# Optimization experiments

Measured on AMD Instinct MI355X. Metric: run time of the kernel, lower is better.

## Reference

```python
import jax, jax.numpy as jnp
import numpy as np

H = 128        # hidden_dim
HEADS = 4      # conv1 heads
NTYPE = 50     # node_type_num
MZN = 32       # model_zoo_num
MAXN = 64      # max_node_num
B = 16         # outer batch
G = B * MZN    # num graphs = 512
N = G * MAXN   # total nodes = 32768
E = N * 8      # edges = 262144


def layer_norm(x, g, b):
    mu = x.mean(-1, keepdims=True)
    var = ((x - mu) ** 2).mean(-1, keepdims=True)
    return (x - mu) / jnp.sqrt(var + 1e-6) * g + b


def gat_conv(x, src, dst, W, a_src, a_dst, bias):
    # PyG GATConv: lin (no bias) -> per-edge LeakyReLU(0.2) scores with
    # self-loops -> segment softmax over dst -> scatter-sum, concat heads + bias.
    n = x.shape[0]
    heads, c = a_src.shape
    xp = (x @ W).reshape(n, heads, c)              # [N,heads,c]
    al_s = (xp * a_src).sum(-1)                    # [N,heads]
    al_d = (xp * a_dst).sum(-1)                    # [N,heads]
    loop = jnp.arange(n)
    s = jnp.concatenate([src, loop])               # add self-loops
    d = jnp.concatenate([dst, loop])
    e = jax.nn.leaky_relu(al_s[s] + al_d[d], 0.2)  # [E+N,heads]
    m = jax.ops.segment_max(e, d, num_segments=n)
    ex = jnp.exp(e - m[d])
    denom = jax.ops.segment_sum(ex, d, num_segments=n)
    alpha = ex / denom[d]                          # segment softmax
    msg = xp[s] * alpha[:, :, None]                # [E+N,heads,c]
    out = jax.ops.segment_sum(msg, d, num_segments=n)
    return out.reshape(n, heads * c) + bias


def setup_inputs() -> dict:
    key = jax.random.key(0)
    ks = jax.random.split(key, 32)
    def rn(k, shape, s=0.05):
        return jax.random.normal(k, shape, jnp.float32) * s
    inp = {
        "t": jax.random.normal(ks[0], (G, 768), jnp.float32),
        "v": jax.random.normal(ks[1], (G, 768), jnp.float32),
        "m_idx": jax.random.randint(ks[2], (N,), 0, NTYPE + 1),
        "edge_index": jax.random.randint(ks[3], (2, E), 0, N),
        "Wt": rn(ks[4], (768, H)), "bt": jnp.zeros((H,), jnp.float32),
        "Wv": rn(ks[5], (768, H)), "bv": jnp.zeros((H,), jnp.float32),
        "emb": rn(ks[6], (NTYPE + 1, H), 1.0),
        "Wnode": rn(ks[7], (H, H)), "bnode": jnp.zeros((H,), jnp.float32),
        "Wstart": rn(ks[8], (2 * H, H)), "bstart": jnp.zeros((H,), jnp.float32),
        "ln_g": jnp.ones((H,), jnp.float32), "ln_b": jnp.zeros((H,), jnp.float32),
        "W1": rn(ks[9], (H, HEADS * H)),
        "a_src1": rn(ks[10], (HEADS, H)), "a_dst1": rn(ks[11], (HEADS, H)),
        "b1": jnp.zeros((HEADS * H,), jnp.float32),
        "W2": rn(ks[12], (HEADS * H, H)),
        "a_src2": rn(ks[13], (1, H)), "a_dst2": rn(ks[14], (1, H)),
        "b2": jnp.zeros((H,), jnp.float32),
        "Wo1": rn(ks[15], (H, H)), "bo1": jnp.zeros((H,), jnp.float32),
        "Wo2": rn(ks[16], (H, 1)), "bo2": jnp.zeros((1,), jnp.float32),
    }
    return inp


def reference(t, v, Wt, bt, Wv, bv, emb, Wnode, bnode, Wstart, bstart, ln_g, ln_b,
              W1, a_src1, a_dst1, b1, W2, a_src2, a_dst2, b2, Wo1, bo1, Wo2, bo2,
              m_idx, edge_index):
    te = t @ Wt + bt                               # [G,H]
    ve = v @ Wv + bv                               # [G,H]
    ne = emb[m_idx].reshape(G, MAXN, H)            # node type embeddings
    ne = ne @ Wnode + bnode
    start = jnp.concatenate([ve, te], axis=-1) @ Wstart + bstart
    ne = ne.at[:, 0].set(start).reshape(N, H)
    x = layer_norm(ne, ln_g, ln_b)
    src, dst = edge_index[0], edge_index[1]
    x = jax.nn.elu(gat_conv(x, src, dst, W1, a_src1, a_dst1, b1))  # [N,4H]
    x = jax.nn.elu(gat_conv(x, src, dst, W2, a_src2, a_dst2, b2))  # [N,H]
    mask = (m_idx >= 1).astype(x.dtype).reshape(G, MAXN, 1)
    pooled = (x.reshape(G, MAXN, H) * mask).sum(1) / mask.sum(1)   # masked mean
    h1 = jax.nn.leaky_relu(pooled.reshape(B, MZN, H) @ Wo1 + bo1, 0.01)
    logits = (h1 @ Wo2 + bo2).reshape(B, MZN)
    return logits
```

## Files before the change

### kernel.cpp

```cpp
#include <hip/hip_runtime.h>
#include <hip/hip_bf16.h>

typedef __hip_bfloat16 bf16;
typedef __attribute__((ext_vector_type(8))) short s8v;
typedef __attribute__((ext_vector_type(4))) float f4v;

#define NN 32768
#define EE 262144
#define GG 512
#define LDW 520

__device__ __forceinline__ float2 unpk(unsigned u) {
  float2 r;
  r.x = __uint_as_float(u << 16);
  r.y = __uint_as_float(u & 0xffff0000u);
  return r;
}
__device__ __forceinline__ unsigned pk(float x, float y) {
  union { bf16 h[2]; unsigned u; } p;
  p.h[0] = __float2bfloat16(x);
  p.h[1] = __float2bfloat16(y);
  return p.u;
}
__device__ __forceinline__ short f2bf_bits(float x) {
  bf16 h = __float2bfloat16(x);
  return *reinterpret_cast<short*>(&h);
}
__device__ __forceinline__ float wred_sum(float v) {
#pragma unroll
  for (int o = 32; o; o >>= 1) v += __shfl_xor(v, o, 64);
  return v;
}

__device__ __forceinline__ void packB_one(const float* W, int N, int K, int id, s8v* Bp) {
  int lane = id & 63;
  int tmp = id >> 6;
  int ksteps = K >> 5;
  int ks = tmp % ksteps;
  int nt = tmp / ksteps;
  int n = nt * 16 + (lane & 15);
  int kbase = ks * 32 + (lane >> 4) * 8;
  s8v r;
#pragma unroll
  for (int j = 0; j < 8; j++) r[j] = f2bf_bits(W[(size_t)(kbase + j) * N + n]);
  Bp[id] = r;
}

__global__ __launch_bounds__(256) void prep_kernel(
    const int* __restrict__ dst, int* __restrict__ indeg,
    const float* __restrict__ W1, s8v* __restrict__ Bp1,
    const float* __restrict__ W2, s8v* __restrict__ Bp2,
    const float* __restrict__ a_src1, const float* __restrict__ a_dst1,
    float* __restrict__ ws1, float* __restrict__ wd1,
    const float* __restrict__ emb, const float* __restrict__ Wnode,
    const float* __restrict__ bnode, bf16* __restrict__ emb2_b,
    const float* __restrict__ Wv, const float* __restrict__ Wt,
    const float* __restrict__ Ws,
    const float* __restrict__ bv, const float* __restrict__ bt,
    const float* __restrict__ bstart,
    float* __restrict__ Wvs, float* __restrict__ Wts,
    float* __restrict__ bs2) {
  int b = blockIdx.x, tid = threadIdx.x;
  if (b < 1024) {
    int e = b * 256 + tid;
    atomicAdd(&indeg[dst[e]], 1);
  } else if (b < 1056) {
    packB_one(W1, 512, 128, (b - 1024) * 256 + tid, Bp1);
  } else if (b < 1088) {
    packB_one(W2, 128, 512, (b - 1056) * 256 + tid, Bp2);
  } else if (b < 1090) {
    int id = (b - 1088) * 256 + tid;
    int h = id >> 7, k = id & 127;
    float s = 0.f, d = 0.f;
    for (int c = 0; c < 128; c++) {
      float w0 = W1[(size_t)k * 512 + h * 128 + c];
      s = fmaf(w0, a_src1[h * 128 + c], s);
      d = fmaf(w0, a_dst1[h * 128 + c], d);
    }
    ws1[id] = s;
    wd1[id] = d;
  } else if (b < 1192) {
    __shared__ float red[256];
    int bb = b - 1090;
    int lo = tid & 63, slice = tid >> 6;
    long oid = (long)bb * 64 + lo;
    bool live = (oid < 51L * 128);
    int m = 0, n = 0;
    if (live) { m = (int)(oid >> 7); n = (int)(oid & 127); }
    float acc = 0.f;
    if (live) {
      const float* Ar = emb + (size_t)m * 128;
      for (int k = slice * 32; k < slice * 32 + 32; k++)
        acc = fmaf(Ar[k], Wnode[(size_t)k * 128 + n], acc);
    }
    red[tid] = acc;
    __syncthreads();
    if (slice == 0 && live) {
      float v = red[lo] + red[64 + lo] + red[128 + lo] + red[192 + lo];
      emb2_b[(size_t)m * 128 + n] = __float2bfloat16(v + bnode[n]);
    }
  } else if (b < 1576) {
    int id = (b - 1192) * 256 + tid;
    bool isT = id >= 49152;
    int o = isT ? id - 49152 : id;
    int k = o >> 6, cp = o & 63, c0 = cp * 2;
    const float* Wrow = (isT ? Wt : Wv) + (size_t)k * 128;
    const float* Wsc = Ws + (isT ? (size_t)128 * 128 : 0);
    float s0 = 0.f, s1 = 0.f;
    for (int j = 0; j < 128; j++) {
      float w = Wrow[j];
      float2 q = *(const float2*)(Wsc + (size_t)j * 128 + c0);
      s0 = fmaf(w, q.x, s0);
      s1 = fmaf(w, q.y, s1);
    }
    float* dp = (isT ? Wts : Wvs) + (size_t)k * 128 + c0;
    dp[0] = s0;
    dp[1] = s1;
  } else {
    if (tid < 128) {
      float s = bstart[tid];
      for (int k = 0; k < 128; k++) {
        s = fmaf(bv[k], Ws[(size_t)k * 128 + tid], s);
        s = fmaf(bt[k], Ws[(size_t)(128 + k) * 128 + tid], s);
      }
      bs2[tid] = s;
    }
  }
}

__global__ __launch_bounds__(1024) void scan_start_kernel(
    const int* __restrict__ indeg, int* __restrict__ off, int* __restrict__ cursor,
    const float* __restrict__ tf, const float* __restrict__ vf,
    const float* __restrict__ Wvs, const float* __restrict__ Wts,
    const float* __restrict__ bs2, bf16* __restrict__ start_b) {
  int t = threadIdx.x;
  if (blockIdx.x == 0) {
    __shared__ int sh[1024];
    int loc[32];
    int s = 0;
    int base = t * 32;
#pragma unroll
    for (int j = 0; j < 32; j++) { loc[j] = indeg[base + j]; s += loc[j]; }
    sh[t] = s;
    __syncthreads();
    for (int d = 1; d < 1024; d <<= 1) {
      int v = (t >= d) ? sh[t - d] : 0;
      __syncthreads();
      sh[t] += v;
      __syncthreads();
    }
    int run = (t == 0) ? 0 : sh[t - 1];
#pragma unroll
    for (int j = 0; j < 32; j++) { off[base + j] = run; cursor[base + j] = run; run += loc[j]; }
    if (t == 1023) off[NN] = run;
    return;
  }
  __shared__ float red[1024];
  int g = blockIdx.x - 1;
  int c = t & 127, slice = t >> 7;
  const float* vrow = vf + (size_t)g * 768;
  const float* trow = tf + (size_t)g * 768;
  float acc = 0.f;
  int k0 = slice * 96;
#pragma unroll 4
  for (int k = k0; k < k0 + 96; k++)
    acc = fmaf(vrow[k], Wvs[(size_t)k * 128 + c], fmaf(trow[k], Wts[(size_t)k * 128 + c], acc));
  red[t] = acc;
  __syncthreads();
  if (t < 512) red[t] += red[t + 512];
  __syncthreads();
  if (t < 256) red[t] += red[t + 256];
  __syncthreads();
  if (t < 128) {
    float s = red[t] + red[t + 128] + bs2[t];
    start_b[(size_t)g * 128 + t] = __float2bfloat16(s);
  }
}

__global__ __launch_bounds__(256) void fill_ln_kernel(
    const int* __restrict__ src, const int* __restrict__ dst,
    int* __restrict__ cursor, int* __restrict__ esrc,
    const unsigned* __restrict__ start_b, const unsigned* __restrict__ emb2_b,
    const int* __restrict__ m_idx, const float* __restrict__ lng,
    const float* __restrict__ lnb, const float* __restrict__ ws1,
    const float* __restrict__ wd1, unsigned* __restrict__ x0b,
    float* __restrict__ als, float* __restrict__ ald) {
  int b = blockIdx.x;
  if (b < 1024) {
    int e = b * 256 + threadIdx.x;
    int p = atomicAdd(&cursor[dst[e]], 1);
    esrc[p] = src[e];
    return;
  }
  int bb = b - 1024;
  int i = bb * 4 + (threadIdx.x >> 6);
  int lane = threadIdx.x & 63;
  int g = i >> 6, n = i & 63;
  const unsigned* row = (n == 0) ? (start_b + (size_t)g * 64) : (emb2_b + (size_t)m_idx[i] * 64);
  float2 v = unpk(row[lane]);
  float mu = wred_sum(v.x + v.y) * (1.f / 128.f);
  float dx = v.x - mu, dy = v.y - mu;
  float var = wred_sum(dx * dx + dy * dy) * (1.f / 128.f);
  float rstd = rsqrtf(var + 1e-6f);
  float2 gg = ((const float2*)lng)[lane];
  float2 bbv = ((const float2*)lnb)[lane];
  float xx = dx * rstd * gg.x + bbv.x;
  float xy = dy * rstd * gg.y + bbv.y;
  x0b[(size_t)i * 64 + lane] = pk(xx, xy);
#pragma unroll
  for (int h = 0; h < 4; h++) {
    float2 s2 = ((const float2*)(ws1 + h * 128))[lane];
    float2 d2 = ((const float2*)(wd1 + h * 128))[lane];
    float ps = wred_sum(xx * s2.x + xy * s2.y);
    float pd = wred_sum(xx * d2.x + xy * d2.y);
    if (lane == 0) { als[i * 4 + h] = ps; ald[i * 4 + h] = pd; }
  }
}

__global__ __launch_bounds__(256) void alpha1_kernel(const float4* __restrict__ als4,
                                                     const float4* __restrict__ ald4,
                                                     const int* __restrict__ off,
                                                     const int* __restrict__ esrc,
                                                     float4* __restrict__ aw4,
                                                     float4* __restrict__ selfw4,
                                                     float4* __restrict__ inv4) {
  int i = blockIdx.x * 256 + threadIdx.x;
  if (i >= NN) return;
  float4 ad = ald4[i];
  float4 as = als4[i];
  float4 sw;
  {
    float v0 = as.x + ad.x, v1 = as.y + ad.y, v2 = as.z + ad.z, v3 = as.w + ad.w;
    v0 = v0 > 0.f ? v0 : 0.2f * v0; v1 = v1 > 0.f ? v1 : 0.2f * v1;
    v2 = v2 > 0.f ? v2 : 0.2f * v2; v3 = v3 > 0.f ? v3 : 0.2f * v3;
    sw = make_float4(__expf(v0), __expf(v1), __expf(v2), __expf(v3));
  }
  float d0 = sw.x, d1 = sw.y, d2 = sw.z, d3 = sw.w;
  int s0 = off[i], s1 = off[i + 1];
  for (int e = s0; e < s1; e++) {
    float4 a = als4[esrc[e]];
    float v0 = a.x + ad.x, v1 = a.y + ad.y, v2 = a.z + ad.z, v3 = a.w + ad.w;
    v0 = v0 > 0.f ? v0 : 0.2f * v0; v1 = v1 > 0.f ? v1 : 0.2f * v1;
    v2 = v2 > 0.f ? v2 : 0.2f * v2; v3 = v3 > 0.f ? v3 : 0.2f * v3;
    v0 = __expf(v0); v1 = __expf(v1); v2 = __expf(v2); v3 = __expf(v3);
    aw4[e] = make_float4(v0, v1, v2, v3);
    d0 += v0; d1 += v1; d2 += v2; d3 += v3;
  }
  selfw4[i] = sw;
  inv4[i] = make_float4(1.f / d0, 1.f / d1, 1.f / d2, 1.f / d3);
}

__global__ __launch_bounds__(256) void alpha2_kernel(const float* __restrict__ als,
                                                     const float* __restrict__ ald,
                                                     const int* __restrict__ off,
                                                     const int* __restrict__ esrc,
                                                     float* __restrict__ aw,
                                                     float* __restrict__ selfw,
                                                     float* __restrict__ inv) {
  int i = blockIdx.x * 256 + threadIdx.x;
  if (i >= NN) return;
  float adi = ald[i];
  float selfSc = als[i] + adi;
  selfSc = selfSc > 0.f ? selfSc : 0.2f * selfSc;
  float sw = __expf(selfSc);
  float denom = sw;
  int s0 = off[i], s1 = off[i + 1];
  for (int e = s0; e < s1; e++) {
    float sc = als[esrc[e]] + adi;
    sc = sc > 0.f ? sc : 0.2f * sc;
    float w = __expf(sc);
    aw[e] = w;
    denom += w;
  }
  selfw[i] = sw;
  inv[i] = 1.f / denom;
}

__global__ __launch_bounds__(256) void conv12f_kernel(
    const uint4* __restrict__ x0,
    const float4* __restrict__ aw4, const float4* __restrict__ selfw4,
    const float4* __restrict__ inv4,
    const int* __restrict__ off, const int* __restrict__ esrc,
    const s8v* __restrict__ Bp1, const float* __restrict__ b1,
    const s8v* __restrict__ Bp2,
    const float* __restrict__ a_src2, const float* __restrict__ a_dst2,
    short* __restrict__ xp2, float* __restrict__ als2, float* __restrict__ ald2) {
  __shared__ short lds[64 * LDW];
  int tid = threadIdx.x;
  int brow = blockIdx.x * 64;
  {
    int c8 = tid & 15, rsub = tid >> 4;
    for (int grp = 0; grp < 4; grp++) {
      int i = brow + grp * 16 + rsub;
      float4 sw = selfw4[i];
      uint4 xv = x0[(size_t)i * 16 + c8];
      float x[8];
      { float2 p0 = unpk(xv.x), p1 = unpk(xv.y), p2 = unpk(xv.z), p3 = unpk(xv.w);
        x[0]=p0.x; x[1]=p0.y; x[2]=p1.x; x[3]=p1.y; x[4]=p2.x; x[5]=p2.y; x[6]=p3.x; x[7]=p3.y; }
      float acc[4][8];
#pragma unroll
      for (int j = 0; j < 8; j++) {
        acc[0][j] = sw.x * x[j]; acc[1][j] = sw.y * x[j];
        acc[2][j] = sw.z * x[j]; acc[3][j] = sw.w * x[j];
      }
      int s0 = off[i], s1 = off[i + 1];
      for (int e = s0; e < s1; e++) {
        int s = esrc[e];
        float4 wv = aw4[e];
        uint4 m = x0[(size_t)s * 16 + c8];
        float2 q0 = unpk(m.x), q1 = unpk(m.y), q2 = unpk(m.z), q3 = unpk(m.w);
        float q[8] = {q0.x, q0.y, q1.x, q1.y, q2.x, q2.y, q3.x, q3.y};
#pragma unroll
        for (int j = 0; j < 8; j++) {
          acc[0][j] = fmaf(wv.x, q[j], acc[0][j]);
          acc[1][j] = fmaf(wv.y, q[j], acc[1][j]);
          acc[2][j] = fmaf(wv.z, q[j], acc[2][j]);
          acc[3][j] = fmaf(wv.w, q[j], acc[3][j]);
        }
      }
      float4 iv = inv4[i];
      float ivh[4] = {iv.x, iv.y, iv.z, iv.w};
      int row = grp * 16 + rsub;
#pragma unroll
      for (int h = 0; h < 4; h++) {
        uint4 o;
        o.x = pk(acc[h][0] * ivh[h], acc[h][1] * ivh[h]);
        o.y = pk(acc[h][2] * ivh[h], acc[h][3] * ivh[h]);
        o.z = pk(acc[h][4] * ivh[h], acc[h][5] * ivh[h]);
        o.w = pk(acc[h][6] * ivh[h], acc[h][7] * ivh[h]);
        *(uint4*)(lds + row * LDW + h * 128 + c8 * 8) = o;
      }
    }
  }
  __syncthreads();
  int wv = tid >> 6, lane = tid & 63, quad = lane >> 4, l16 = lane & 15;
  int arow = (wv * 16 + l16) * LDW;
  for (int h = 0; h < 4; h++) {
    f4v acc[8] = {};
#pragma unroll
    for (int ks = 0; ks < 4; ks++) {
      s8v a = *(const s8v*)(lds + arow + h * 128 + ks * 32 + quad * 8);
#pragma unroll
      for (int nt = 0; nt < 8; nt++) {
        s8v bf = Bp1[(size_t)((h * 8 + nt) * 4 + ks) * 64 + lane];
        acc[nt] = __builtin_amdgcn_mfma_f32_16x16x32_bf16(a, bf, acc[nt], 0, 0, 0);
      }
    }
#pragma unroll
    for (int nt = 0; nt < 8; nt++) {
      float bb = b1[h * 128 + nt * 16 + l16];
#pragma unroll
      for (int r = 0; r < 4; r++) {
        float vv = acc[nt][r] + bb;
        vv = vv > 0.f ? vv : (__expf(vv) - 1.f);
        lds[(wv * 16 + quad * 4 + r) * LDW + h * 128 + nt * 16 + l16] = f2bf_bits(vv);
      }
    }
  }
  __syncthreads();
  f4v acc2[8] = {};
  for (int ks = 0; ks < 16; ks++) {
    s8v a = *(const s8v*)(lds + arow + ks * 32 + quad * 8);
#pragma unroll
    for (int nt = 0; nt < 8; nt++) {
      s8v bf = Bp2[(size_t)(nt * 16 + ks) * 64 + lane];
      acc2[nt] = __builtin_amdgcn_mfma_f32_16x16x32_bf16(a, bf, acc2[nt], 0, 0, 0);
    }
  }
#pragma unroll
  for (int nt = 0; nt < 8; nt++)
#pragma unroll
    for (int r = 0; r < 4; r++)
      lds[(wv * 16 + quad * 4 + r) * LDW + nt * 16 + l16] = f2bf_bits(acc2[nt][r]);
  float2 as = ((const float2*)a_src2)[lane];
  float2 ad = ((const float2*)a_dst2)[lane];
  for (int r = 0; r < 16; r++) {
    int row = wv * 16 + r;
    float2 x = unpk(*(const unsigned*)(lds + row * LDW + lane * 2));
    float ps = wred_sum(x.x * as.x + x.y * as.y);
    float pd = wred_sum(x.x * ad.x + x.y * ad.y);
    if (lane == 0) { als2[brow + row] = ps; ald2[brow + row] = pd; }
  }
  __syncthreads();
#pragma unroll
  for (int rep = 0; rep < 4; rep++) {
    int idx = rep * 256 + tid;
    int row = idx >> 4, c16 = idx & 15;
    uint4 val = *(const uint4*)(lds + row * LDW + c16 * 8);
    *(uint4*)(xp2 + (size_t)(brow + row) * 128 + c16 * 8) = val;
  }
}

__global__ __launch_bounds__(256) void tail2_kernel(
    const uint4* __restrict__ xp,
    const float* __restrict__ aw, const float* __restrict__ selfw,
    const float* __restrict__ inv,
    const int* __restrict__ off, const int* __restrict__ esrc,
    const float* __restrict__ b2, const int* __restrict__ m_idx,
    const float* __restrict__ Wo1, const float* __restrict__ bo1,
    const float* __restrict__ Wo2, const float* __restrict__ bo2,
    float* __restrict__ out) {
  __shared__ float x2t[64 * 132];
  __shared__ float maskf[64];
  __shared__ float pl[128];
  __shared__ float red[256];
  int g = blockIdx.x, tid = threadIdx.x;
  if (tid < 64) maskf[tid] = (m_idx[g * 64 + tid] >= 1) ? 1.f : 0.f;
  int c8 = tid & 15, rsub = tid >> 4;
  for (int grp = 0; grp < 4; grp++) {
    int i = g * 64 + grp * 16 + rsub;
    float sw = selfw[i];
    float ivv = inv[i];
    uint4 xv = xp[(size_t)i * 16 + c8];
    float2 p0 = unpk(xv.x), p1 = unpk(xv.y), p2 = unpk(xv.z), p3 = unpk(xv.w);
    float a0 = sw * p0.x, a1 = sw * p0.y, a2 = sw * p1.x, a3 = sw * p1.y;
    float a4 = sw * p2.x, a5 = sw * p2.y, a6 = sw * p3.x, a7 = sw * p3.y;
    int s0 = off[i], s1 = off[i + 1];
    int e = s0;
    for (; e + 1 < s1; e += 2) {
      int sA = esrc[e], sB = esrc[e + 1];
      float wA = aw[e], wB = aw[e + 1];
      uint4 mA = xp[(size_t)sA * 16 + c8];
      uint4 mB = xp[(size_t)sB * 16 + c8];
      float2 q0 = unpk(mA.x), q1 = unpk(mA.y), q2 = unpk(mA.z), q3 = unpk(mA.w);
      a0 = fmaf(wA, q0.x, a0); a1 = fmaf(wA, q0.y, a1);
      a2 = fmaf(wA, q1.x, a2); a3 = fmaf(wA, q1.y, a3);
      a4 = fmaf(wA, q2.x, a4); a5 = fmaf(wA, q2.y, a5);
      a6 = fmaf(wA, q3.x, a6); a7 = fmaf(wA, q3.y, a7);
      q0 = unpk(mB.x); q1 = unpk(mB.y); q2 = unpk(mB.z); q3 = unpk(mB.w);
      a0 = fmaf(wB, q0.x, a0); a1 = fmaf(wB, q0.y, a1);
      a2 = fmaf(wB, q1.x, a2); a3 = fmaf(wB, q1.y, a3);
      a4 = fmaf(wB, q2.x, a4); a5 = fmaf(wB, q2.y, a5);
      a6 = fmaf(wB, q3.x, a6); a7 = fmaf(wB, q3.y, a7);
    }
    if (e < s1) {
      int sA = esrc[e];
      float wA = aw[e];
      uint4 mA = xp[(size_t)sA * 16 + c8];
      float2 q0 = unpk(mA.x), q1 = unpk(mA.y), q2 = unpk(mA.z), q3 = unpk(mA.w);
      a0 = fmaf(wA, q0.x, a0); a1 = fmaf(wA, q0.y, a1);
      a2 = fmaf(wA, q1.x, a2); a3 = fmaf(wA, q1.y, a3);
      a4 = fmaf(wA, q2.x, a4); a5 = fmaf(wA, q2.y, a5);
      a6 = fmaf(wA, q3.x, a6); a7 = fmaf(wA, q3.y, a7);
    }
    float4 bb0 = ((const float4*)b2)[c8 * 2];
    float4 bb1 = ((const float4*)b2)[c8 * 2 + 1];
    a0 = a0 * ivv + bb0.x; a1 = a1 * ivv + bb0.y; a2 = a2 * ivv + bb0.z; a3 = a3 * ivv + bb0.w;
    a4 = a4 * ivv + bb1.x; a5 = a5 * ivv + bb1.y; a6 = a6 * ivv + bb1.z; a7 = a7 * ivv + bb1.w;
    a0 = a0 > 0.f ? a0 : (__expf(a0) - 1.f);
    a1 = a1 > 0.f ? a1 : (__expf(a1) - 1.f);
    a2 = a2 > 0.f ? a2 : (__expf(a2) - 1.f);
    a3 = a3 > 0.f ? a3 : (__expf(a3) - 1.f);
    a4 = a4 > 0.f ? a4 : (__expf(a4) - 1.f);
    a5 = a5 > 0.f ? a5 : (__expf(a5) - 1.f);
    a6 = a6 > 0.f ? a6 : (__expf(a6) - 1.f);
    a7 = a7 > 0.f ? a7 : (__expf(a7) - 1.f);
    float* dp = x2t + (grp * 16 + rsub) * 132 + c8 * 8;
    dp[0] = a0; dp[1] = a1; dp[2] = a2; dp[3] = a3;
    dp[4] = a4; dp[5] = a5; dp[6] = a6; dp[7] = a7;
  }
  __syncthreads();
  int c = tid & 127, half = tid >> 7;
  float pacc = 0.f;
  for (int n = half * 32; n < half * 32 + 32; n++) pacc += maskf[n] * x2t[n * 132 + c];
  red[tid] = pacc;
  __syncthreads();
  float cnt = 0.f;
  for (int n = 0; n < 64; n++) cnt += maskf[n];
  if (half == 0) pl[c] = (red[c] + red[c + 128]) / cnt;
  __syncthreads();
  float hacc = 0.f;
  for (int k = half * 64; k < half * 64 + 64; k++)
    hacc = fmaf(pl[k], Wo1[(size_t)k * 128 + c], hacc);
  red[tid] = hacc;
  __syncthreads();
  if (half == 0) {
    float hh = red[c] + red[c + 128] + bo1[c];
    hh = hh > 0.f ? hh : 0.01f * hh;
    red[c] = hh * Wo2[c];
  }
  __syncthreads();
  for (int d = 64; d; d >>= 1) {
    if (tid < d) red[tid] += red[tid + d];
    __syncthreads();
  }
  if (tid == 0) out[g] = red[0] + bo2[0];
}

extern "C" void kernel_launch(void* const* d_in, const int* in_sizes, int n_in, void* d_out,
                              int out_size, void* d_ws, size_t ws_size, hipStream_t stream) {
  (void)n_in; (void)out_size; (void)ws_size;
  bool dict_order = (in_sizes[2] == NN);
  int IM, IE, IF[25];
  if (dict_order) {
    IM = 2; IE = 3;
    const int f[25] = {0, 1, 4, 5, 6, 7, 8, 9, 10, 11, 12, 13, 14, 15, 16, 17, 18,
                       19, 20, 21, 22, 23, 24, 25, 26};
    for (int k = 0; k < 25; k++) IF[k] = f[k];
  } else {
    IM = 25; IE = 26;
    for (int k = 0; k < 25; k++) IF[k] = k;
  }
  const int* m_idx = (const int*)d_in[IM];
  const int* eidx = (const int*)d_in[IE];
  float* out = (float*)d_out;
  const int* e_src = eidx;
  const int* e_dst = eidx + EE;

  const float* t = (const float*)d_in[IF[0]];
  const float* v = (const float*)d_in[IF[1]];
  const float* Wt = (const float*)d_in[IF[2]];     const float* bt = (const float*)d_in[IF[3]];
  const float* Wv = (const float*)d_in[IF[4]];     const float* bv = (const float*)d_in[IF[5]];
  const float* emb = (const float*)d_in[IF[6]];
  const float* Wnode = (const float*)d_in[IF[7]];  const float* bnode = (const float*)d_in[IF[8]];
  const float* Wstart = (const float*)d_in[IF[9]]; const float* bstart = (const float*)d_in[IF[10]];
  const float* ln_g = (const float*)d_in[IF[11]];  const float* ln_b = (const float*)d_in[IF[12]];
  const float* W1 = (const float*)d_in[IF[13]];
  const float* a_src1 = (const float*)d_in[IF[14]]; const float* a_dst1 = (const float*)d_in[IF[15]];
  const float* b1 = (const float*)d_in[IF[16]];
  const float* W2 = (const float*)d_in[IF[17]];
  const float* a_src2 = (const float*)d_in[IF[18]]; const float* a_dst2 = (const float*)d_in[IF[19]];
  const float* b2 = (const float*)d_in[IF[20]];
  const float* Wo1 = (const float*)d_in[IF[21]];   const float* bo1 = (const float*)d_in[IF[22]];
  const float* Wo2 = (const float*)d_in[IF[23]];   const float* bo2 = (const float*)d_in[IF[24]];

  char* w = (char*)d_ws;
  bf16* x0b = (bf16*)w;
  bf16* xp2b = (bf16*)(w + ((size_t)8 << 20));
  size_t so = (size_t)16 << 20;
  bf16* emb2_b = (bf16*)(w + so); so += 51 * 128 * 2 + 256;
  bf16* start_b = (bf16*)(w + so); so += 512 * 128 * 2;
  float* als1 = (float*)(w + so); so += NN * 4 * 4;
  float* ald1 = (float*)(w + so); so += NN * 4 * 4;
  float* als2 = (float*)(w + so); so += NN * 4;
  float* ald2 = (float*)(w + so); so += NN * 4;
  float* aw1 = (float*)(w + so); so += EE * 4 * 4;
  float* selfw1 = (float*)(w + so); so += NN * 4 * 4;
  float* inv1 = (float*)(w + so); so += NN * 4 * 4;
  float* aw2 = (float*)(w + so); so += EE * 4;
  float* selfw2 = (float*)(w + so); so += NN * 4;
  float* inv2 = (float*)(w + so); so += NN * 4;
  float* ws1 = (float*)(w + so); so += 512 * 4;
  float* wd1 = (float*)(w + so); so += 512 * 4;
  float* Wvs = (float*)(w + so); so += 768 * 128 * 4;
  float* Wts = (float*)(w + so); so += 768 * 128 * 4;
  float* bs2 = (float*)(w + so); so += 512;
  int* indeg = (int*)(w + so); so += NN * 4;
  int* csroff = (int*)(w + so); so += (NN + 1) * 4 + 252;
  int* cursor = (int*)(w + so); so += NN * 4;
  int* esrc = (int*)(w + so); so += EE * 4;
  s8v* Bp1 = (s8v*)(w + so); so += 32 * 4 * 64 * 16;
  s8v* Bp2 = (s8v*)(w + so); so += 8 * 16 * 64 * 16;

  hipMemsetAsync(indeg, 0, NN * 4, stream);
  prep_kernel<<<1577, 256, 0, stream>>>(e_dst, indeg,
      W1, Bp1, W2, Bp2, a_src1, a_dst1, ws1, wd1,
      emb, Wnode, bnode, emb2_b,
      Wv, Wt, Wstart, bv, bt, bstart, Wvs, Wts, bs2);
  scan_start_kernel<<<513, 1024, 0, stream>>>(indeg, csroff, cursor,
      t, v, Wvs, Wts, bs2, start_b);
  fill_ln_kernel<<<9216, 256, 0, stream>>>(e_src, e_dst, cursor, esrc,
      (const unsigned*)start_b, (const unsigned*)emb2_b, m_idx, ln_g, ln_b,
      ws1, wd1, (unsigned*)x0b, als1, ald1);
  alpha1_kernel<<<NN / 256, 256, 0, stream>>>((const float4*)als1, (const float4*)ald1,
                                              csroff, esrc, (float4*)aw1,
                                              (float4*)selfw1, (float4*)inv1);
  conv12f_kernel<<<NN / 64, 256, 0, stream>>>((const uint4*)x0b,
      (const float4*)aw1, (const float4*)selfw1, (const float4*)inv1,
      csroff, esrc, Bp1, b1, Bp2, a_src2, a_dst2, (short*)xp2b, als2, ald2);
  alpha2_kernel<<<NN / 256, 256, 0, stream>>>(als2, ald2, csroff, esrc, aw2, selfw2, inv2);
  tail2_kernel<<<GG, 256, 0, stream>>>((const uint4*)xp2b, aw2, selfw2, inv2,
      csroff, esrc, b2, m_idx, Wo1, bo1, Wo2, bo2, out);
}
```

Measured before the change: 315.0 us.

## Compute edge attention scores per-edge and fold softmax denominators into aggregation

```diff
diff --git a/kernel.cpp b/kernel.cpp
--- a/kernel.cpp
+++ b/kernel.cpp
@@ -179,7 +179,7 @@
 
 __global__ __launch_bounds__(256) void fill_ln_kernel(
     const int* __restrict__ src, const int* __restrict__ dst,
-    int* __restrict__ cursor, int* __restrict__ esrc,
+    int* __restrict__ cursor, int* __restrict__ esrc, int* __restrict__ edst,
     const unsigned* __restrict__ start_b, const unsigned* __restrict__ emb2_b,
     const int* __restrict__ m_idx, const float* __restrict__ lng,
     const float* __restrict__ lnb, const float* __restrict__ ws1,
@@ -188,8 +188,10 @@
   int b = blockIdx.x;
   if (b < 1024) {
     int e = b * 256 + threadIdx.x;
-    int p = atomicAdd(&cursor[dst[e]], 1);
+    int d = dst[e];
+    int p = atomicAdd(&cursor[d], 1);
     esrc[p] = src[e];
+    edst[p] = d;
     return;
   }
   int bb = b - 1024;
@@ -217,69 +219,33 @@
   }
 }
 
-__global__ __launch_bounds__(256) void alpha1_kernel(const float4* __restrict__ als4,
-                                                     const float4* __restrict__ ald4,
-                                                     const int* __restrict__ off,
-                                                     const int* __restrict__ esrc,
-                                                     float4* __restrict__ aw4,
-                                                     float4* __restrict__ selfw4,
-                                                     float4* __restrict__ inv4) {
-  int i = blockIdx.x * 256 + threadIdx.x;
-  if (i >= NN) return;
-  float4 ad = ald4[i];
-  float4 as = als4[i];
-  float4 sw;
-  {
-    float v0 = as.x + ad.x, v1 = as.y + ad.y, v2 = as.z + ad.z, v3 = as.w + ad.w;
-    v0 = v0 > 0.f ? v0 : 0.2f * v0; v1 = v1 > 0.f ? v1 : 0.2f * v1;
-    v2 = v2 > 0.f ? v2 : 0.2f * v2; v3 = v3 > 0.f ? v3 : 0.2f * v3;
-    sw = make_float4(__expf(v0), __expf(v1), __expf(v2), __expf(v3));
-  }
-  float d0 = sw.x, d1 = sw.y, d2 = sw.z, d3 = sw.w;
-  int s0 = off[i], s1 = off[i + 1];
-  for (int e = s0; e < s1; e++) {
-    float4 a = als4[esrc[e]];
-    float v0 = a.x + ad.x, v1 = a.y + ad.y, v2 = a.z + ad.z, v3 = a.w + ad.w;
-    v0 = v0 > 0.f ? v0 : 0.2f * v0; v1 = v1 > 0.f ? v1 : 0.2f * v1;
-    v2 = v2 > 0.f ? v2 : 0.2f * v2; v3 = v3 > 0.f ? v3 : 0.2f * v3;
-    v0 = __expf(v0); v1 = __expf(v1); v2 = __expf(v2); v3 = __expf(v3);
-    aw4[e] = make_float4(v0, v1, v2, v3);
-    d0 += v0; d1 += v1; d2 += v2; d3 += v3;
-  }
-  selfw4[i] = sw;
-  inv4[i] = make_float4(1.f / d0, 1.f / d1, 1.f / d2, 1.f / d3);
-}
-
-__global__ __launch_bounds__(256) void alpha2_kernel(const float* __restrict__ als,
-                                                     const float* __restrict__ ald,
-                                                     const int* __restrict__ off,
-                                                     const int* __restrict__ esrc,
-                                                     float* __restrict__ aw,
-                                                     float* __restrict__ selfw,
-                                                     float* __restrict__ inv) {
-  int i = blockIdx.x * 256 + threadIdx.x;
-  if (i >= NN) return;
-  float adi = ald[i];
-  float selfSc = als[i] + adi;
-  selfSc = selfSc > 0.f ? selfSc : 0.2f * selfSc;
-  float sw = __expf(selfSc);
-  float denom = sw;
-  int s0 = off[i], s1 = off[i + 1];
-  for (int e = s0; e < s1; e++) {
-    float sc = als[esrc[e]] + adi;
-    sc = sc > 0.f ? sc : 0.2f * sc;
-    float w = __expf(sc);
-    aw[e] = w;
-    denom += w;
-  }
-  selfw[i] = sw;
-  inv[i] = 1.f / denom;
+__global__ __launch_bounds__(256) void escore1_kernel(
+    const float4* __restrict__ als4, const float4* __restrict__ ald4,
+    const int* __restrict__ esrc, const int* __restrict__ edst,
+    float4* __restrict__ aw4) {
+  int p = blockIdx.x * 256 + threadIdx.x;
+  float4 a = als4[esrc[p]];
+  float4 d = ald4[edst[p]];
+  float v0 = a.x + d.x, v1 = a.y + d.y, v2 = a.z + d.z, v3 = a.w + d.w;
+  v0 = v0 > 0.f ? v0 : 0.2f * v0; v1 = v1 > 0.f ? v1 : 0.2f * v1;
+  v2 = v2 > 0.f ? v2 : 0.2f * v2; v3 = v3 > 0.f ? v3 : 0.2f * v3;
+  aw4[p] = make_float4(__expf(v0), __expf(v1), __expf(v2), __expf(v3));
+}
+
+__global__ __launch_bounds__(256) void escore2_kernel(
+    const float* __restrict__ als, const float* __restrict__ ald,
+    const int* __restrict__ esrc, const int* __restrict__ edst,
+    float* __restrict__ aw) {
+  int p = blockIdx.x * 256 + threadIdx.x;
+  float sc = als[esrc[p]] + ald[edst[p]];
+  sc = sc > 0.f ? sc : 0.2f * sc;
+  aw[p] = __expf(sc);
 }
 
 __global__ __launch_bounds__(256) void conv12f_kernel(
     const uint4* __restrict__ x0,
-    const float4* __restrict__ aw4, const float4* __restrict__ selfw4,
-    const float4* __restrict__ inv4,
+    const float4* __restrict__ aw4,
+    const float4* __restrict__ als4, const float4* __restrict__ ald4,
     const int* __restrict__ off, const int* __restrict__ esrc,
     const s8v* __restrict__ Bp1, const float* __restrict__ b1,
     const s8v* __restrict__ Bp2,
@@ -292,7 +258,12 @@
     int c8 = tid & 15, rsub = tid >> 4;
     for (int grp = 0; grp < 4; grp++) {
       int i = brow + grp * 16 + rsub;
-      float4 sw = selfw4[i];
+      float4 sa = als4[i], sd = ald4[i];
+      float u0 = sa.x + sd.x, u1 = sa.y + sd.y, u2 = sa.z + sd.z, u3 = sa.w + sd.w;
+      u0 = u0 > 0.f ? u0 : 0.2f * u0; u1 = u1 > 0.f ? u1 : 0.2f * u1;
+      u2 = u2 > 0.f ? u2 : 0.2f * u2; u3 = u3 > 0.f ? u3 : 0.2f * u3;
+      float sw0 = __expf(u0), sw1 = __expf(u1), sw2 = __expf(u2), sw3 = __expf(u3);
+      float dn0 = sw0, dn1 = sw1, dn2 = sw2, dn3 = sw3;
       uint4 xv = x0[(size_t)i * 16 + c8];
       float x[8];
       { float2 p0 = unpk(xv.x), p1 = unpk(xv.y), p2 = unpk(xv.z), p3 = unpk(xv.w);
@@ -300,26 +271,53 @@
       float acc[4][8];
 #pragma unroll
       for (int j = 0; j < 8; j++) {
-        acc[0][j] = sw.x * x[j]; acc[1][j] = sw.y * x[j];
-        acc[2][j] = sw.z * x[j]; acc[3][j] = sw.w * x[j];
-      }
-      int s0 = off[i], s1 = off[i + 1];
-      for (int e = s0; e < s1; e++) {
-        int s = esrc[e];
-        float4 wv = aw4[e];
-        uint4 m = x0[(size_t)s * 16 + c8];
-        float2 q0 = unpk(m.x), q1 = unpk(m.y), q2 = unpk(m.z), q3 = unpk(m.w);
-        float q[8] = {q0.x, q0.y, q1.x, q1.y, q2.x, q2.y, q3.x, q3.y};
+        acc[0][j] = sw0 * x[j]; acc[1][j] = sw1 * x[j];
+        acc[2][j] = sw2 * x[j]; acc[3][j] = sw3 * x[j];
+      }
+      int e0 = off[i], e1 = off[i + 1];
+      int e = e0;
+      for (; e + 1 < e1; e += 2) {
+        int sA = esrc[e], sB = esrc[e + 1];
+        float4 wA = aw4[e], wB = aw4[e + 1];
+        uint4 mA = x0[(size_t)sA * 16 + c8];
+        uint4 mB = x0[(size_t)sB * 16 + c8];
+        float2 q0 = unpk(mA.x), q1 = unpk(mA.y), q2 = unpk(mA.z), q3 = unpk(mA.w);
+        float qa[8] = {q0.x, q0.y, q1.x, q1.y, q2.x, q2.y, q3.x, q3.y};
 #pragma unroll
         for (int j = 0; j < 8; j++) {
-          acc[0][j] = fmaf(wv.x, q[j], acc[0][j]);
-          acc[1][j] = fmaf(wv.y, q[j], acc[1][j]);
-          acc[2][j] = fmaf(wv.z, q[j], acc[2][j]);
-          acc[3][j] = fmaf(wv.w, q[j], acc[3][j]);
+          acc[0][j] = fmaf(wA.x, qa[j], acc[0][j]);
+          acc[1][j] = fmaf(wA.y, qa[j], acc[1][j]);
+          acc[2][j] = fmaf(wA.z, qa[j], acc[2][j]);
+          acc[3][j] = fmaf(wA.w, qa[j], acc[3][j]);
         }
-      }
-      float4 iv = inv4[i];
-      float ivh[4] = {iv.x, iv.y, iv.z, iv.w};
+        dn0 += wA.x; dn1 += wA.y; dn2 += wA.z; dn3 += wA.w;
+        q0 = unpk(mB.x); q1 = unpk(mB.y); q2 = unpk(mB.z); q3 = unpk(mB.w);
+        float qb[8] = {q0.x, q0.y, q1.x, q1.y, q2.x, q2.y, q3.x, q3.y};
+#pragma unroll
+        for (int j = 0; j < 8; j++) {
+          acc[0][j] = fmaf(wB.x, qb[j], acc[0][j]);
+          acc[1][j] = fmaf(wB.y, qb[j], acc[1][j]);
+          acc[2][j] = fmaf(wB.z, qb[j], acc[2][j]);
+          acc[3][j] = fmaf(wB.w, qb[j], acc[3][j]);
+        }
+        dn0 += wB.x; dn1 += wB.y; dn2 += wB.z; dn3 += wB.w;
+      }
+      if (e < e1) {
+        int sA = esrc[e];
+        float4 wA = aw4[e];
+        uint4 mA = x0[(size_t)sA * 16 + c8];
+        float2 q0 = unpk(mA.x), q1 = unpk(mA.y), q2 = unpk(mA.z), q3 = unpk(mA.w);
+        float qa[8] = {q0.x, q0.y, q1.x, q1.y, q2.x, q2.y, q3.x, q3.y};
+#pragma unroll
+        for (int j = 0; j < 8; j++) {
+          acc[0][j] = fmaf(wA.x, qa[j], acc[0][j]);
+          acc[1][j] = fmaf(wA.y, qa[j], acc[1][j]);
+          acc[2][j] = fmaf(wA.z, qa[j], acc[2][j]);
+          acc[3][j] = fmaf(wA.w, qa[j], acc[3][j]);
+        }
+        dn0 += wA.x; dn1 += wA.y; dn2 += wA.z; dn3 += wA.w;
+      }
+      float ivh[4] = {1.f / dn0, 1.f / dn1, 1.f / dn2, 1.f / dn3};
       int row = grp * 16 + rsub;
 #pragma unroll
       for (int h = 0; h < 4; h++) {
@@ -393,8 +391,8 @@
 
 __global__ __launch_bounds__(256) void tail2_kernel(
     const uint4* __restrict__ xp,
-    const float* __restrict__ aw, const float* __restrict__ selfw,
-    const float* __restrict__ inv,
+    const float* __restrict__ aw,
+    const float* __restrict__ als, const float* __restrict__ ald,
     const int* __restrict__ off, const int* __restrict__ esrc,
     const float* __restrict__ b2, const int* __restrict__ m_idx,
     const float* __restrict__ Wo1, const float* __restrict__ bo1,
@@ -409,8 +407,10 @@
   int c8 = tid & 15, rsub = tid >> 4;
   for (int grp = 0; grp < 4; grp++) {
     int i = g * 64 + grp * 16 + rsub;
-    float sw = selfw[i];
-    float ivv = inv[i];
+    float selfSc = als[i] + ald[i];
+    selfSc = selfSc > 0.f ? selfSc : 0.2f * selfSc;
+    float sw = __expf(selfSc);
+    float dnm = sw;
     uint4 xv = xp[(size_t)i * 16 + c8];
     float2 p0 = unpk(xv.x), p1 = unpk(xv.y), p2 = unpk(xv.z), p3 = unpk(xv.w);
     float a0 = sw * p0.x, a1 = sw * p0.y, a2 = sw * p1.x, a3 = sw * p1.y;
@@ -427,11 +427,13 @@
       a2 = fmaf(wA, q1.x, a2); a3 = fmaf(wA, q1.y, a3);
       a4 = fmaf(wA, q2.x, a4); a5 = fmaf(wA, q2.y, a5);
       a6 = fmaf(wA, q3.x, a6); a7 = fmaf(wA, q3.y, a7);
+      dnm += wA;
       q0 = unpk(mB.x); q1 = unpk(mB.y); q2 = unpk(mB.z); q3 = unpk(mB.w);
       a0 = fmaf(wB, q0.x, a0); a1 = fmaf(wB, q0.y, a1);
       a2 = fmaf(wB, q1.x, a2); a3 = fmaf(wB, q1.y, a3);
       a4 = fmaf(wB, q2.x, a4); a5 = fmaf(wB, q2.y, a5);
       a6 = fmaf(wB, q3.x, a6); a7 = fmaf(wB, q3.y, a7);
+      dnm += wB;
     }
     if (e < s1) {
       int sA = esrc[e];
@@ -442,7 +444,9 @@
       a2 = fmaf(wA, q1.x, a2); a3 = fmaf(wA, q1.y, a3);
       a4 = fmaf(wA, q2.x, a4); a5 = fmaf(wA, q2.y, a5);
       a6 = fmaf(wA, q3.x, a6); a7 = fmaf(wA, q3.y, a7);
-    }
+      dnm += wA;
+    }
+    float ivv = 1.f / dnm;
     float4 bb0 = ((const float4*)b2)[c8 * 2];
     float4 bb1 = ((const float4*)b2)[c8 * 2 + 1];
     a0 = a0 * ivv + bb0.x; a1 = a1 * ivv + bb0.y; a2 = a2 * ivv + bb0.z; a3 = a3 * ivv + bb0.w;
@@ -535,11 +539,7 @@
   float* als2 = (float*)(w + so); so += NN * 4;
   float* ald2 = (float*)(w + so); so += NN * 4;
   float* aw1 = (float*)(w + so); so += EE * 4 * 4;
-  float* selfw1 = (float*)(w + so); so += NN * 4 * 4;
-  float* inv1 = (float*)(w + so); so += NN * 4 * 4;
   float* aw2 = (float*)(w + so); so += EE * 4;
-  float* selfw2 = (float*)(w + so); so += NN * 4;
-  float* inv2 = (float*)(w + so); so += NN * 4;
   float* ws1 = (float*)(w + so); so += 512 * 4;
   float* wd1 = (float*)(w + so); so += 512 * 4;
   float* Wvs = (float*)(w + so); so += 768 * 128 * 4;
@@ -549,6 +549,7 @@
   int* csroff = (int*)(w + so); so += (NN + 1) * 4 + 252;
   int* cursor = (int*)(w + so); so += NN * 4;
   int* esrc = (int*)(w + so); so += EE * 4;
+  int* edst = (int*)(w + so); so += EE * 4;
   s8v* Bp1 = (s8v*)(w + so); so += 32 * 4 * 64 * 16;
   s8v* Bp2 = (s8v*)(w + so); so += 8 * 16 * 64 * 16;
 
@@ -559,16 +560,15 @@
       Wv, Wt, Wstart, bv, bt, bstart, Wvs, Wts, bs2);
   scan_start_kernel<<<513, 1024, 0, stream>>>(indeg, csroff, cursor,
       t, v, Wvs, Wts, bs2, start_b);
-  fill_ln_kernel<<<9216, 256, 0, stream>>>(e_src, e_dst, cursor, esrc,
+  fill_ln_kernel<<<9216, 256, 0, stream>>>(e_src, e_dst, cursor, esrc, edst,
       (const unsigned*)start_b, (const unsigned*)emb2_b, m_idx, ln_g, ln_b,
       ws1, wd1, (unsigned*)x0b, als1, ald1);
-  alpha1_kernel<<<NN / 256, 256, 0, stream>>>((const float4*)als1, (const float4*)ald1,
-                                              csroff, esrc, (float4*)aw1,
-                                              (float4*)selfw1, (float4*)inv1);
+  escore1_kernel<<<EE / 256, 256, 0, stream>>>((const float4*)als1, (const float4*)ald1,
+                                               esrc, edst, (float4*)aw1);
   conv12f_kernel<<<NN / 64, 256, 0, stream>>>((const uint4*)x0b,
-      (const float4*)aw1, (const float4*)selfw1, (const float4*)inv1,
+      (const float4*)aw1, (const float4*)als1, (const float4*)ald1,
       csroff, esrc, Bp1, b1, Bp2, a_src2, a_dst2, (short*)xp2b, als2, ald2);
-  alpha2_kernel<<<NN / 256, 256, 0, stream>>>(als2, ald2, csroff, esrc, aw2, selfw2, inv2);
-  tail2_kernel<<<GG, 256, 0, stream>>>((const uint4*)xp2b, aw2, selfw2, inv2,
+  escore2_kernel<<<EE / 256, 256, 0, stream>>>(als2, ald2, esrc, edst, aw2);
+  tail2_kernel<<<GG, 256, 0, stream>>>((const uint4*)xp2b, aw2, als2, ald2,
       csroff, esrc, b2, m_idx, Wo1, bo1, Wo2, bo2, out);
 }
```

Measured after the change: 293.5 us. 6.8% less time.
